# Kernel tuning notes

Hardware: AMD Instinct MI355X
Metric: run time of the kernel (lower is better)

Reference implementation:

```python
import jax, jax.numpy as jnp
import numpy as np

HC = 4            # hc_mult
HIDDEN = 4096
SINKHORN_ITERS = 5
HC_EPS = 1e-5
NORM_EPS = 1e-6
B, S = 2, 4096


def setup_inputs() -> dict:
    key = jax.random.key(0)
    k0, k1, k2, k3 = jax.random.split(key, 4)
    mix = (2 + HC) * HC  # 24
    return {
        "hidden_streams": jax.random.normal(k0, (B, S, HC, HIDDEN), dtype=jnp.float32),
        # small init so sigmoid/softmax gates stay in a sane range
        "fn": jax.random.normal(k1, (mix, HC * HIDDEN), dtype=jnp.float32) * 0.01,
        "base": jax.random.normal(k2, (mix,), dtype=jnp.float32),
        "scale": jax.random.normal(k3, (3,), dtype=jnp.float32),
    }


def reference(hidden_streams, fn, base, scale):
    hc = HC
    # flatten streams: [B, S, hc*hidden]
    flat = hidden_streams.reshape(hidden_streams.shape[0], hidden_streams.shape[1], -1).astype(jnp.float32)
    rsqrt = jax.lax.rsqrt(jnp.mean(jnp.square(flat), axis=-1, keepdims=True) + NORM_EPS)
    # packed projection to mix=(2+hc)*hc gate logits, RMS-scaled
    mix = jnp.einsum("bsd,md->bsm", flat, fn.astype(jnp.float32)) * rsqrt
    pre_scale, post_scale, comb_scale = scale[0], scale[1], scale[2]
    pre = jax.nn.sigmoid(mix[..., :hc] * pre_scale + base[:hc]) + HC_EPS
    post = 2.0 * jax.nn.sigmoid(mix[..., hc:2 * hc] * post_scale + base[hc:2 * hc])
    comb_logit = mix[..., 2 * hc:].reshape(*mix.shape[:-1], hc, hc) * comb_scale + base[2 * hc:].reshape(hc, hc)
    comb = jax.nn.softmax(comb_logit, axis=-1) + HC_EPS
    comb = comb / (jnp.sum(comb, axis=-2, keepdims=True) + HC_EPS)
    for _ in range(SINKHORN_ITERS - 1):
        comb = comb / (jnp.sum(comb, axis=-1, keepdims=True) + HC_EPS)
        comb = comb / (jnp.sum(comb, axis=-2, keepdims=True) + HC_EPS)
    return pre, post, comb
```

## Files before the change

### kernel.cpp

```cpp
#include <hip/hip_runtime.h>
#include <hip/hip_bf16.h>
#include <math.h>
#include <stdint.h>

#define HC 4
#define DIM 16384
#define MIXN 24
#define NROWS 8192
#define KSPLIT 32
#define KSL 512
#define NSTEPS 16
#define NSTREAM 32
#define ROWS_PER_STREAM 256
#define NTILES 16
#define THREADS1 512
#define HC_EPS 1e-5f
#define NORM_EPS 1e-6f

#define PRE_OFF 0
#define POST_OFF (NROWS * HC)
#define COMB_OFF (2 * NROWS * HC)

typedef float f32x4 __attribute__((ext_vector_type(4)));
typedef float accf4 __attribute__((ext_vector_type(4)));
typedef short bf16x8 __attribute__((ext_vector_type(8)));
typedef short bf16x4 __attribute__((ext_vector_type(4)));

__device__ __forceinline__ short f2bf(float x) {
    union { __hip_bfloat16 h; short s; } u;
    u.h = __float2bfloat16(x);
    return u.s;
}

__global__ __launch_bounds__(THREADS1) void hyper_k1(
    const float* __restrict__ hs,
    const float* __restrict__ fn,
    float* __restrict__ ws)
{
    const int tid  = threadIdx.x;
    const int wave = tid >> 6;
    const int lane = tid & 63;
    const int l15  = lane & 15;
    const int kg   = lane >> 4;
    const int ks     = blockIdx.x & (KSPLIT - 1);
    const int stream = blockIdx.x >> 5;

    __shared__ __align__(16) short s_fn[2][NSTEPS][512];
    __shared__ __align__(16) short s_a[2][NSTEPS][512];
    __shared__ float sC[8][400];

    #pragma unroll 1
    for (int p = 0; p < 4; ++p) {
        const int idx  = p * THREADS1 + tid;
        const int kgf  = idx & 3;
        const int s    = (idx >> 2) & 15;
        const int c    = (idx >> 6) & 15;
        const int tile = idx >> 10;
        const int col  = tile ? (c + 8) : c;
        const float* g = fn + (size_t)col * DIM + ks * KSL + s * 32 + kgf * 8;
        const f32x4 v0 = *(const f32x4*)g;
        const f32x4 v1 = *(const f32x4*)(g + 4);
        bf16x8 b = { f2bf(v0.x), f2bf(v0.y), f2bf(v0.z), f2bf(v0.w),
                     f2bf(v1.x), f2bf(v1.y), f2bf(v1.z), f2bf(v1.w) };
        *(bf16x8*)&s_fn[tile][s][(kgf * 16 + c) * 8] = b;
    }
    __syncthreads();

    const int st_slo = lane >> 3;
    const int st_kg  = (lane >> 1) & 3;
    const int st_e   = (lane & 1) * 4;
    const int sr0 = 2 * wave, sr1 = 2 * wave + 1;

    f32x4 R0, R1, R2, R3;

#define ISSUE(T) do { \
    const float* g0 = hs + (size_t)(stream * ROWS_PER_STREAM + (T) * 16 + sr0) * DIM + ks * KSL; \
    const float* g1 = hs + (size_t)(stream * ROWS_PER_STREAM + (T) * 16 + sr1) * DIM + ks * KSL; \
    R0 = *(const f32x4*)(g0 +   0 + lane * 4); \
    R1 = *(const f32x4*)(g0 + 256 + lane * 4); \
    R2 = *(const f32x4*)(g1 +   0 + lane * 4); \
    R3 = *(const f32x4*)(g1 + 256 + lane * 4); \
} while (0)

#define WR1(B, Rj, r, j) do { \
    const int s_ = (j) * 8 + st_slo; \
    int byte_ = ((s_ * 64 + st_kg * 16 + (r)) * 16) + st_e * 2; \
    byte_ ^= ((s_ & 7) << 4); \
    bf16x4 v_ = { f2bf(Rj.x), f2bf(Rj.y), f2bf(Rj.z), f2bf(Rj.w) }; \
    *(bf16x4*)((char*)(&s_a[B][0][0]) + byte_) = v_; \
} while (0)

#define WRALL(B) do { \
    WR1(B, R0, sr0, 0); WR1(B, R1, sr0, 1); \
    WR1(B, R2, sr1, 0); WR1(B, R3, sr1, 1); \
} while (0)

    ISSUE(0);
    asm volatile("s_waitcnt vmcnt(0)" ::: "memory");
    WRALL(0);
    ISSUE(1);

    #pragma unroll 1
    for (int t = 0; t < NTILES; ++t) {
        const int buf = t & 1;
        asm volatile("s_waitcnt lgkmcnt(0)" ::: "memory");
        __builtin_amdgcn_s_barrier();
        __builtin_amdgcn_sched_barrier(0);

        accf4 acc0 = {0.f, 0.f, 0.f, 0.f};
        accf4 acc1 = {0.f, 0.f, 0.f, 0.f};
        accf4 accS = {0.f, 0.f, 0.f, 0.f};
        #pragma unroll
        for (int i = 0; i < 2; ++i) {
            const int s = wave * 2 + i;
            int ab = ((s * 64 + lane) * 16) ^ ((s & 7) << 4);
            const bf16x8 af = *(const bf16x8*)((const char*)(&s_a[buf][0][0]) + ab);
            const bf16x8 b0 = *(const bf16x8*)&s_fn[0][s][lane * 8];
            const bf16x8 b1 = *(const bf16x8*)&s_fn[1][s][lane * 8];
            acc0 = __builtin_amdgcn_mfma_f32_16x16x32_bf16(af, b0, acc0, 0, 0, 0);
            acc1 = __builtin_amdgcn_mfma_f32_16x16x32_bf16(af, b1, acc1, 0, 0, 0);
            accS = __builtin_amdgcn_mfma_f32_16x16x32_bf16(af, af, accS, 0, 0, 0);
        }

        #pragma unroll
        for (int i = 0; i < 4; ++i)
            sC[wave][(kg * 4 + i) * 25 + l15] = acc0[i];
        if (l15 >= 8) {
            #pragma unroll
            for (int i = 0; i < 4; ++i)
                sC[wave][(kg * 4 + i) * 25 + l15 + 8] = acc1[i];
        }
        #pragma unroll
        for (int i = 0; i < 4; ++i)
            if (l15 == kg * 4 + i) sC[wave][l15 * 25 + 24] = accS[i];

        asm volatile("s_waitcnt lgkmcnt(0)" ::: "memory");
        __builtin_amdgcn_s_barrier();
        __builtin_amdgcn_sched_barrier(0);

        if (tid < 400) {
            const float v = sC[0][tid] + sC[1][tid] + sC[2][tid] + sC[3][tid]
                          + sC[4][tid] + sC[5][tid] + sC[6][tid] + sC[7][tid];
            ws[((size_t)(stream * NTILES + t) * KSPLIT + ks) * 400 + tid] = v;
        }

        if (t + 1 < NTILES) {
            asm volatile("s_waitcnt vmcnt(1)" ::: "memory");
            WRALL((t + 1) & 1);
            if (t + 2 < NTILES) ISSUE(t + 2);
        }
    }
#undef ISSUE
#undef WR1
#undef WRALL
}

__global__ __launch_bounds__(256) void hyper_k2(
    const float* __restrict__ ws,
    const float* __restrict__ base,
    const float* __restrict__ scale,
    float* __restrict__ out)
{
    const int r  = blockIdx.x * 256 + threadIdx.x;
    const int rt = r >> 4, rr = r & 15;

    float v[25];
    #pragma unroll
    for (int c = 0; c < 25; ++c) v[c] = 0.f;
    #pragma unroll 1
    for (int ks = 0; ks < KSPLIT; ++ks) {
        const float* w = ws + ((size_t)rt * KSPLIT + ks) * 400 + rr * 25;
        #pragma unroll
        for (int c = 0; c < 25; ++c) v[c] += w[c];
    }

    const float rs = 1.0f / sqrtf(v[24] * (1.0f / (float)DIM) + NORM_EPS);
    const float s0 = scale[0], s1 = scale[1], s2 = scale[2];

    #pragma unroll
    for (int i = 0; i < HC; ++i) {
        const float z = v[i] * rs * s0 + base[i];
        out[PRE_OFF + r * HC + i] = 1.0f / (1.0f + expf(-z)) + HC_EPS;
    }
    #pragma unroll
    for (int i = 0; i < HC; ++i) {
        const float z = v[HC + i] * rs * s1 + base[HC + i];
        out[POST_OFF + r * HC + i] = 2.0f / (1.0f + expf(-z));
    }

    float c[HC][HC];
    #pragma unroll
    for (int i = 0; i < HC; ++i) {
        float l[HC];
        #pragma unroll
        for (int j = 0; j < HC; ++j)
            l[j] = v[2 * HC + i * HC + j] * rs * s2 + base[2 * HC + i * HC + j];
        const float mx = fmaxf(fmaxf(l[0], l[1]), fmaxf(l[2], l[3]));
        float e[HC];
        float sum = 0.0f;
        #pragma unroll
        for (int j = 0; j < HC; ++j) { e[j] = expf(l[j] - mx); sum += e[j]; }
        const float inv = 1.0f / sum;
        #pragma unroll
        for (int j = 0; j < HC; ++j) c[i][j] = e[j] * inv + HC_EPS;
    }
    #pragma unroll
    for (int j = 0; j < HC; ++j) {
        const float cs = c[0][j] + c[1][j] + c[2][j] + c[3][j] + HC_EPS;
        const float inv = 1.0f / cs;
        c[0][j] *= inv; c[1][j] *= inv; c[2][j] *= inv; c[3][j] *= inv;
    }
    #pragma unroll
    for (int it = 0; it < 4; ++it) {
        #pragma unroll
        for (int i = 0; i < HC; ++i) {
            const float rsum = c[i][0] + c[i][1] + c[i][2] + c[i][3] + HC_EPS;
            const float inv = 1.0f / rsum;
            c[i][0] *= inv; c[i][1] *= inv; c[i][2] *= inv; c[i][3] *= inv;
        }
        #pragma unroll
        for (int j = 0; j < HC; ++j) {
            const float cs = c[0][j] + c[1][j] + c[2][j] + c[3][j] + HC_EPS;
            const float inv = 1.0f / cs;
            c[0][j] *= inv; c[1][j] *= inv; c[2][j] *= inv; c[3][j] *= inv;
        }
    }
    #pragma unroll
    for (int i = 0; i < HC; ++i)
        #pragma unroll
        for (int j = 0; j < HC; ++j)
            out[COMB_OFF + r * (HC * HC) + i * HC + j] = c[i][j];
}

extern "C" void kernel_launch(void* const* d_in, const int* in_sizes, int n_in,
                              void* d_out, int out_size, void* d_ws, size_t ws_size,
                              hipStream_t stream) {
    const float* hs    = (const float*)d_in[0];
    const float* fn    = (const float*)d_in[1];
    const float* base  = (const float*)d_in[2];
    const float* scale = (const float*)d_in[3];
    float* out = (float*)d_out;
    float* ws  = (float*)d_ws;

    hyper_k1<<<KSPLIT * NSTREAM, THREADS1, 0, stream>>>(hs, fn, ws);
    hyper_k2<<<NROWS / 256, 256, 0, stream>>>(ws, base, scale, out);
}
```

Before: 145.5 us.

## Deepen global-load prefetch to two tiles with triple-buffered LDS and fewer blocks

The grid shrinks from 32 to 8 row-streams per k-slice (256 blocks instead of 1024), so each block now walks 64 row tiles instead of 16. Global loads are issued two tiles ahead using two alternating register sets, and the LDS staging for the A operand becomes a ring of three buffers. The explicit vmcnt waits are removed and the compiler is left to insert waits before registers are used. This aims to hide more HBM latency per block and amortize the per-block fn conversion, at the cost of far fewer blocks (possibly under one wave of blocks per CU) and more registers.

```diff
diff --git a/kernel.cpp b/kernel.cpp
--- a/kernel.cpp
+++ b/kernel.cpp
@@ -10,9 +10,10 @@
 #define KSPLIT 32
 #define KSL 512
 #define NSTEPS 16
-#define NSTREAM 32
-#define ROWS_PER_STREAM 256
-#define NTILES 16
+#define NSTREAM 8
+#define ROWS_PER_STREAM 1024
+#define NTILES 64
+#define NBUF 3
 #define THREADS1 512
 #define HC_EPS 1e-5f
 #define NORM_EPS 1e-6f
@@ -46,7 +47,7 @@
     const int stream = blockIdx.x >> 5;
 
     __shared__ __align__(16) short s_fn[2][NSTEPS][512];
-    __shared__ __align__(16) short s_a[2][NSTEPS][512];
+    __shared__ __align__(16) short s_a[NBUF][NSTEPS][512];
     __shared__ float sC[8][400];
 
     #pragma unroll 1
@@ -71,38 +72,39 @@
     const int st_e   = (lane & 1) * 4;
     const int sr0 = 2 * wave, sr1 = 2 * wave + 1;
 
-    f32x4 R0, R1, R2, R3;
-
-#define ISSUE(T) do { \
+    f32x4 RA0, RA1, RA2, RA3;
+    f32x4 RB0, RB1, RB2, RB3;
+
+#define ISSUE(P0, P1, P2, P3, T) do { \
     const float* g0 = hs + (size_t)(stream * ROWS_PER_STREAM + (T) * 16 + sr0) * DIM + ks * KSL; \
     const float* g1 = hs + (size_t)(stream * ROWS_PER_STREAM + (T) * 16 + sr1) * DIM + ks * KSL; \
-    R0 = *(const f32x4*)(g0 +   0 + lane * 4); \
-    R1 = *(const f32x4*)(g0 + 256 + lane * 4); \
-    R2 = *(const f32x4*)(g1 +   0 + lane * 4); \
-    R3 = *(const f32x4*)(g1 + 256 + lane * 4); \
+    P0 = *(const f32x4*)(g0 +   0 + lane * 4); \
+    P1 = *(const f32x4*)(g0 + 256 + lane * 4); \
+    P2 = *(const f32x4*)(g1 +   0 + lane * 4); \
+    P3 = *(const f32x4*)(g1 + 256 + lane * 4); \
 } while (0)
 
-#define WR1(B, Rj, r, j) do { \
+#define WR1(BUF, Rj, r, j) do { \
     const int s_ = (j) * 8 + st_slo; \
     int byte_ = ((s_ * 64 + st_kg * 16 + (r)) * 16) + st_e * 2; \
     byte_ ^= ((s_ & 7) << 4); \
     bf16x4 v_ = { f2bf(Rj.x), f2bf(Rj.y), f2bf(Rj.z), f2bf(Rj.w) }; \
-    *(bf16x4*)((char*)(&s_a[B][0][0]) + byte_) = v_; \
+    *(bf16x4*)((char*)(&s_a[BUF][0][0]) + byte_) = v_; \
 } while (0)
 
-#define WRALL(B) do { \
-    WR1(B, R0, sr0, 0); WR1(B, R1, sr0, 1); \
-    WR1(B, R2, sr1, 0); WR1(B, R3, sr1, 1); \
+#define WRALL(BUF, P0, P1, P2, P3) do { \
+    WR1(BUF, P0, sr0, 0); WR1(BUF, P1, sr0, 1); \
+    WR1(BUF, P2, sr1, 0); WR1(BUF, P3, sr1, 1); \
 } while (0)
 
-    ISSUE(0);
-    asm volatile("s_waitcnt vmcnt(0)" ::: "memory");
-    WRALL(0);
-    ISSUE(1);
-
-    #pragma unroll 1
+    ISSUE(RA0, RA1, RA2, RA3, 0);
+    ISSUE(RB0, RB1, RB2, RB3, 1);
+    WRALL(0, RA0, RA1, RA2, RA3);
+    ISSUE(RA0, RA1, RA2, RA3, 2);
+
+    int buf = 0;
+    #pragma unroll 2
     for (int t = 0; t < NTILES; ++t) {
-        const int buf = t & 1;
         asm volatile("s_waitcnt lgkmcnt(0)" ::: "memory");
         __builtin_amdgcn_s_barrier();
         __builtin_amdgcn_sched_barrier(0);
@@ -145,10 +147,16 @@
         }
 
         if (t + 1 < NTILES) {
-            asm volatile("s_waitcnt vmcnt(1)" ::: "memory");
-            WRALL((t + 1) & 1);
-            if (t + 2 < NTILES) ISSUE(t + 2);
-        }
+            const int nbuf = (buf + 1 == NBUF) ? 0 : buf + 1;
+            if ((t & 1) == 0) {
+                WRALL(nbuf, RB0, RB1, RB2, RB3);
+                if (t + 3 < NTILES) ISSUE(RB0, RB1, RB2, RB3, t + 3);
+            } else {
+                WRALL(nbuf, RA0, RA1, RA2, RA3);
+                if (t + 3 < NTILES) ISSUE(RA0, RA1, RA2, RA3, t + 3);
+            }
+        }
+        buf = (buf + 1 == NBUF) ? 0 : buf + 1;
     }
 #undef ISSUE
 #undef WR1
```

Result: faster. 133.5 us (-8.3%).
